# Kernel tuning notes

Measured on AMD Instinct MI355X. Metric: run time of the kernel, lower is better.

The kernel has to match this reference:

```python
import jax, jax.numpy as jnp
import numpy as np
import math

NEG_INF = -1e9  # keras Softmax masking uses a large negative additive constant

def setup_inputs() -> dict:
    key = jax.random.key(0)
    k1, k2, k3, k4 = jax.random.split(key, 4)
    B, T, C, H = 4, 4096, 1024, 128
    x = jax.random.normal(k1, (B, T, C), dtype=jnp.float32)
    Wq = jax.random.normal(k2, (C, H), dtype=jnp.float32) * (1.0 / math.sqrt(C))
    Wk = jax.random.normal(k3, (C, H), dtype=jnp.float32) * (1.0 / math.sqrt(C))
    Wv = jax.random.normal(k4, (C, H), dtype=jnp.float32) * (1.0 / math.sqrt(C))
    return {"x": x, "Wq": Wq, "Wk": Wk, "Wv": Wv}

def reference(x, Wq, Wk, Wv):
    # x: [B, T, C]; projections are bias-free Dense layers
    B, T, C = x.shape
    q = jnp.einsum('btc,ch->bth', x, Wq)  # [B, T, H]
    k = jnp.einsum('btc,ch->bth', x, Wk)  # [B, T, H]
    v = jnp.einsum('btc,ch->bth', x, Wv)  # [B, T, H]
    # NOTE: original scales by sqrt(C) (the input channel dim), not sqrt(head_size)
    wei = jnp.einsum('bth,bsh->bts', q, k) / math.sqrt(C)  # [B, T, T]
    causal = jnp.tril(jnp.ones((T, T), dtype=bool))
    wei = jnp.where(causal[None, :, :], wei, NEG_INF)
    wei = jax.nn.softmax(wei, axis=-1)
    # dropout is identity at inference
    out = jnp.einsum('bts,bsh->bth', wei, v)  # [B, T, H]
    return out
```

## Files before the change

kernel.cpp:

```cpp
#include <hip/hip_runtime.h>
#include <hip/hip_bf16.h>

typedef __bf16 bf16x8 __attribute__((ext_vector_type(8)));
typedef __bf16 bf16x4 __attribute__((ext_vector_type(4)));
typedef float  f32x4  __attribute__((ext_vector_type(4)));

#define NB 4
#define TT 4096
#define CC 1024
#define HH 128
#define PS 72
#define MNEG -30000.0f

__device__ inline void gload16(const void* g, void* l) {
  __builtin_amdgcn_global_load_lds(
      (const __attribute__((address_space(1))) void*)g,
      (__attribute__((address_space(3))) void*)l, 16, 0, 0);
}

__global__ void detect_dtype(const unsigned int* __restrict__ xw, int* __restrict__ flag) {
  int t = threadIdx.x;
  int cnt = 0;
#pragma unroll
  for (int i = 0; i < 4; ++i) {
    unsigned int w = xw[t + 64 * i];
    int e = (int)((w >> 7) & 0xFFu);
    cnt += (e >= 100 && e <= 135) ? 1 : 0;
  }
  cnt += __shfl_xor(cnt, 1);  cnt += __shfl_xor(cnt, 2);  cnt += __shfl_xor(cnt, 4);
  cnt += __shfl_xor(cnt, 8);  cnt += __shfl_xor(cnt, 16); cnt += __shfl_xor(cnt, 32);
  if (t == 0) *flag = (cnt >= 128) ? 1 : 0;
}

__global__ __launch_bounds__(256) void transpose_w3(
    const void* __restrict__ Wq, const void* __restrict__ Wk,
    const void* __restrict__ Wv, __bf16* __restrict__ Wt,
    const int* __restrict__ flagp) {
  int isbf = *flagp;
  int which = blockIdx.y;
  const void* W = (which == 0) ? Wq : (which == 1) ? Wk : Wv;
  int idx = blockIdx.x * 256 + threadIdx.x;
  int h = idx & 127, c = idx >> 7;
  __bf16 val;
  if (isbf) val = ((const __bf16*)W)[c * HH + h];
  else      val = (__bf16)(((const float*)W)[c * HH + h]);
  size_t o = (size_t)(c >> 6) * 24576 + (size_t)which * 8192 +
             (size_t)((c >> 3) & 7) * 1024 + (size_t)h * 8 + (c & 7);
  Wt[o] = val;
}

__global__ __launch_bounds__(768) void qkv_proj(
    const void* __restrict__ x, const __bf16* __restrict__ Wt,
    __bf16* __restrict__ q, __bf16* __restrict__ ktl, __bf16* __restrict__ vtl,
    const int* __restrict__ flagp) {
  __shared__ __align__(16) __bf16 XT[2][4096];
  __shared__ __align__(16) __bf16 WTs[2][24576];
  int isbf = *flagp;
  int tid = threadIdx.x, lane = tid & 63, wave = tid >> 6;
  int which = wave >> 2, rowgrp = wave & 3;
  int l16 = lane & 15, quad = lane >> 4;
  int row0 = blockIdx.x * 64;
  f32x4 acc[8] = {};

#define STAGE(ss, b)                                                          \
  for (int i = wave; i < 56; i += 12) {                                       \
    if (i < 8) {                                                              \
      int row = i * 8 + (lane >> 3), g = lane & 7;                            \
      bf16x8 pk;                                                              \
      if (isbf) {                                                             \
        pk = *(const bf16x8*)((const __bf16*)x + (size_t)(row0 + row) * CC +  \
                              (ss) * 64 + g * 8);                             \
      } else {                                                                \
        const float* xf = (const float*)x + (size_t)(row0 + row) * CC +       \
                          (ss) * 64 + g * 8;                                  \
        f32x4 lo = *(const f32x4*)xf;                                         \
        f32x4 hi = *(const f32x4*)(xf + 4);                                   \
        for (int j = 0; j < 4; ++j) { pk[j] = (__bf16)lo[j]; pk[j+4] = (__bf16)hi[j]; } \
      }                                                                       \
      *(bf16x8*)(&XT[b][g * 512 + (row ^ g) * 8]) = pk;                       \
    } else {                                                                  \
      int j = i - 8;                                                          \
      gload16(Wt + (size_t)(ss) * 24576 + j * 512 + lane * 8,                 \
              &WTs[b][j * 512]);                                              \
    }                                                                         \
  }

  STAGE(0, 0);
  for (int s = 0; s < 16; ++s) {
    int cb = s & 1;
    __syncthreads();
    if (s + 1 < 16) { STAGE(s + 1, cb ^ 1); }
#pragma unroll
    for (int t = 0; t < 2; ++t) {
      int g = t * 4 + quad;
      bf16x8 a = *(const bf16x8*)(&XT[cb][g * 512 + ((rowgrp * 16 + l16) ^ g) * 8]);
#pragma unroll
      for (int nt = 0; nt < 8; ++nt) {
        bf16x8 b = *(const bf16x8*)(&WTs[cb][(size_t)which * 8192 + g * 1024 + (nt * 16 + l16) * 8]);
        acc[nt] = __builtin_amdgcn_mfma_f32_16x16x32_bf16(a, b, acc[nt], 0, 0, 0);
      }
    }
  }
#undef STAGE

  int tile = row0 >> 6;
  if (which == 0) {
#pragma unroll
    for (int nt = 0; nt < 8; ++nt)
#pragma unroll
      for (int r = 0; r < 4; ++r) {
        int row = row0 + rowgrp * 16 + quad * 4 + r;
        q[(size_t)row * HH + nt * 16 + l16] = (__bf16)acc[nt][r];
      }
  } else if (which == 1) {
    __bf16* kb = ktl + (size_t)tile * 8192;
#pragma unroll
    for (int nt = 0; nt < 8; ++nt) {
      int h = nt * 16 + l16, g = h >> 3, j = h & 7;
#pragma unroll
      for (int r = 0; r < 4; ++r) {
        int sidx = rowgrp * 16 + quad * 4 + r;
        kb[g * 512 + sidx * 8 + j] = (__bf16)acc[nt][r];
      }
    }
  } else {
    __bf16* vb = vtl + (size_t)tile * 8192;
#pragma unroll
    for (int nt = 0; nt < 8; ++nt) {
      int h = nt * 16 + l16;
      int sb = rowgrp * 16 + quad * 4;
      bf16x4 pk;
#pragma unroll
      for (int r = 0; r < 4; ++r) pk[r] = (__bf16)acc[nt][r];
      *(bf16x4*)(vb + (sb >> 3) * 1024 + h * 8 + (sb & 7)) = pk;
    }
  }
}

__global__ __launch_bounds__(768, 3) void flash_attn(
    const __bf16* __restrict__ q, const __bf16* __restrict__ ktl,
    const __bf16* __restrict__ vtl, void* __restrict__ out,
    const int* __restrict__ flagp) {
  __shared__ __align__(16) __bf16 PL[12][16 * PS];
  __shared__ float CMB[4][32][132];
  __shared__ float CL[4][32];

  int bx = blockIdx.x;
  int batch = (bx & 7) >> 1;
  int qt0 = ((bx >> 3) << 1) | (bx & 1);

  int tid = threadIdx.x, lane = tid & 63, wave = tid >> 6;
  int p = wave >> 1, rowgrp = wave & 1;
  int l16 = lane & 15, quad = lane >> 4;

  int kA = (6 * (qt0 + 1) + 32) / 65;
  kA = max(1, min(5, kA));
  int unit, kg, nkg, qtu, rh;
  if (p < kA) { unit = 0; kg = p;      nkg = kA;     qtu = qt0;      rh = 0; }
  else        { unit = 1; kg = p - kA; nkg = 6 - kA; qtu = 63 - qt0; rh = 1; }

  int qb = qtu * 64;
  int rb = rh * 32 + rowgrp * 16;
  const __bf16* qp  = q   + (size_t)batch * TT * HH;
  const __bf16* ktb = ktl + (size_t)batch * TT * HH;
  const __bf16* vtb = vtl + (size_t)batch * TT * HH;

  bf16x8 qf[4];
  {
    const __bf16* qrow = qp + (size_t)(qb + rb + l16) * HH + quad * 8;
#pragma unroll
    for (int ks = 0; ks < 4; ++ks) qf[ks] = *(const bf16x8*)(qrow + ks * 32);
  }
  bf16x8 onesf;
#pragma unroll
  for (int j = 0; j < 8; ++j) onesf[j] = (l16 == 0) ? (__bf16)1.0f : (__bf16)0.0f;

  f32x4 acc_o[8] = {};
  f32x4 acc_l = {};
  const float SC = 0.0450842200278f;
  const float M0 = 4.0f;
  int qrl = qb + rb + quad * 4;

  for (int jt = kg; jt <= qtu; jt += nkg) {
    const __bf16* kt  = ktb + (size_t)jt * 8192;
    const __bf16* vt2 = vtb + (size_t)jt * 8192;

    bf16x8 kf[4][4];
#pragma unroll
    for (int ks = 0; ks < 4; ++ks)
#pragma unroll
      for (int kn = 0; kn < 4; ++kn)
        kf[ks][kn] = *(const bf16x8*)(kt + ((4 * ks + quad) * 64 + kn * 16 + l16) * 8);

    f32x4 accs[4] = {};
#pragma unroll
    for (int ks = 0; ks < 4; ++ks)
#pragma unroll
      for (int kn = 0; kn < 4; ++kn)
        accs[kn] = __builtin_amdgcn_mfma_f32_16x16x32_bf16(qf[ks], kf[ks][kn], accs[kn], 0, 0, 0);

    bf16x8 vf[2][8];
#pragma unroll
    for (int ks2 = 0; ks2 < 2; ++ks2)
#pragma unroll
      for (int nt = 0; nt < 8; ++nt)
        vf[ks2][nt] = *(const bf16x8*)(vt2 + (ks2 * 4 + quad) * 1024 + (nt * 16 + l16) * 8);

    float pv[4][4];
    if (jt == qtu) {
#pragma unroll
      for (int nt = 0; nt < 4; ++nt) {
        int kcol = jt * 64 + nt * 16 + l16;
#pragma unroll
        for (int r = 0; r < 4; ++r) {
          float z = fmaf(accs[nt][r], SC, -M0);
          z = (kcol <= qrl + r) ? z : MNEG;
          pv[nt][r] = exp2f(z);
        }
      }
    } else {
#pragma unroll
      for (int nt = 0; nt < 4; ++nt)
#pragma unroll
        for (int r = 0; r < 4; ++r)
          pv[nt][r] = exp2f(fmaf(accs[nt][r], SC, -M0));
    }

    __bf16* pw = &PL[wave][0];
#pragma unroll
    for (int nt = 0; nt < 4; ++nt)
#pragma unroll
      for (int r = 0; r < 4; ++r)
        pw[(quad * 4 + r) * PS + nt * 16 + l16] = (__bf16)pv[nt][r];

#pragma unroll
    for (int ks2 = 0; ks2 < 2; ++ks2) {
      bf16x8 pa = *(const bf16x8*)(pw + l16 * PS + ks2 * 32 + quad * 8);
      acc_l = __builtin_amdgcn_mfma_f32_16x16x32_bf16(pa, onesf, acc_l, 0, 0, 0);
#pragma unroll
      for (int nt = 0; nt < 8; ++nt)
        acc_o[nt] = __builtin_amdgcn_mfma_f32_16x16x32_bf16(pa, vf[ks2][nt], acc_o[nt], 0, 0, 0);
    }
  }

  int rr = rowgrp * 16 + quad * 4;
  if (kg > 0) {
    int slot = (unit == 0) ? (kg - 1) : (kA - 1 + kg - 1);
#pragma unroll
    for (int nt = 0; nt < 8; ++nt)
#pragma unroll
      for (int r = 0; r < 4; ++r)
        CMB[slot][rr + r][nt * 16 + l16] = acc_o[nt][r];
    if (l16 == 0) {
#pragma unroll
      for (int r = 0; r < 4; ++r) CL[slot][rr + r] = acc_l[r];
    }
  }
  __syncthreads();
  if (kg == 0) {
    int lo  = (unit == 0) ? 0 : kA - 1;
    int cnt = (unit == 0) ? kA - 1 : 5 - kA;
    int isbf = *flagp;
    __bf16* ob = (__bf16*)out + (size_t)batch * TT * HH;
    float*  of = (float*)out  + (size_t)batch * TT * HH;
    float inv[4];
#pragma unroll
    for (int r = 0; r < 4; ++r) {
      float lr = __shfl(acc_l[r], lane & 48);
      for (int c = 0; c < cnt; ++c) lr += CL[lo + c][rr + r];
      inv[r] = 1.f / fmaxf(lr, 1e-30f);
    }
#pragma unroll
    for (int nt = 0; nt < 8; ++nt)
#pragma unroll
      for (int r = 0; r < 4; ++r) {
        int row = qb + rh * 32 + rr + r;
        int col = nt * 16 + l16;
        float val = acc_o[nt][r];
        for (int c = 0; c < cnt; ++c) val += CMB[lo + c][rr + r][col];
        val *= inv[r];
        size_t idx = (size_t)row * HH + col;
        if (isbf) ob[idx] = (__bf16)val;
        else      of[idx] = val;
      }
  }
}

extern "C" void kernel_launch(void* const* d_in, const int* in_sizes, int n_in,
                              void* d_out, int out_size, void* d_ws, size_t ws_size,
                              hipStream_t stream) {
  const void* x  = d_in[0];
  const void* Wq = d_in[1];
  const void* Wk = d_in[2];
  const void* Wv = d_in[3];
  char* wsb = (char*)d_ws;
  __bf16* q   = (__bf16*)wsb;
  __bf16* ktl = q   + (size_t)NB * TT * HH;
  __bf16* vtl = ktl + (size_t)NB * TT * HH;
  __bf16* wt  = vtl + (size_t)NB * TT * HH;
  size_t base = (((size_t)(3 * NB * TT * HH + 3 * CC * HH) * 2) + 255) & ~(size_t)255;
  int* flag = (int*)(wsb + base);
  (void)ws_size; (void)in_sizes; (void)n_in; (void)out_size;

  detect_dtype<<<1, 64, 0, stream>>>((const unsigned int*)x, flag);
  transpose_w3<<<dim3(512, 3), 256, 0, stream>>>(Wq, Wk, Wv, wt, flag);
  qkv_proj<<<256, 768, 0, stream>>>(x, wt, q, ktl, vtl, flag);
  flash_attn<<<NB * 64, 768, 0, stream>>>(q, ktl, vtl, d_out, flag);
}
```

Before: 175.3 us.

## Split wave pair work by key columns and head halves with shared P tile

Each pair of waves now covers all 32 query rows but splits the S tile's key columns and the output head dimension in half. Each wave loads only half the K and V fragments per tile and shares the P tile through double-buffered LDS, with a __syncthreads per iteration. The loop now runs a uniform trip count across the block, with masked zero-contribution iterations for waves that have fewer tiles. This is meant to halve per-wave global K/V fragment traffic and register pressure, at the cost of block-wide barriers and some wasted padded iterations.

```diff
diff --git a/kernel.cpp b/kernel.cpp
--- a/kernel.cpp
+++ b/kernel.cpp
@@ -141,7 +141,7 @@
     const __bf16* __restrict__ q, const __bf16* __restrict__ ktl,
     const __bf16* __restrict__ vtl, void* __restrict__ out,
     const int* __restrict__ flagp) {
-  __shared__ __align__(16) __bf16 PL[12][16 * PS];
+  __shared__ __align__(16) __bf16 PLs[6][2][32 * PS];
   __shared__ float CMB[4][32][132];
   __shared__ float CL[4][32];
 
@@ -150,110 +150,142 @@
   int qt0 = ((bx >> 3) << 1) | (bx & 1);
 
   int tid = threadIdx.x, lane = tid & 63, wave = tid >> 6;
-  int p = wave >> 1, rowgrp = wave & 1;
+  int p = wave >> 1, rw = wave & 1;
   int l16 = lane & 15, quad = lane >> 4;
 
   int kA = (6 * (qt0 + 1) + 32) / 65;
   kA = max(1, min(5, kA));
-  int unit, kg, nkg, qtu, rh;
-  if (p < kA) { unit = 0; kg = p;      nkg = kA;     qtu = qt0;      rh = 0; }
-  else        { unit = 1; kg = p - kA; nkg = 6 - kA; qtu = 63 - qt0; rh = 1; }
+  int qtB = 63 - qt0;
+  int unit, kg, nkg, qtu, rbase;
+  if (p < kA) { unit = 0; kg = p;      nkg = kA;     qtu = qt0; rbase = 0;  }
+  else        { unit = 1; kg = p - kA; nkg = 6 - kA; qtu = qtB; rbase = 32; }
 
   int qb = qtu * 64;
-  int rb = rh * 32 + rowgrp * 16;
+  int MAXT = max(qt0 / kA + 1, qtB / (6 - kA) + 1);
+  int mytrips = (qtu - kg) / nkg + 1;
+
   const __bf16* qp  = q   + (size_t)batch * TT * HH;
   const __bf16* ktb = ktl + (size_t)batch * TT * HH;
   const __bf16* vtb = vtl + (size_t)batch * TT * HH;
 
-  bf16x8 qf[4];
-  {
-    const __bf16* qrow = qp + (size_t)(qb + rb + l16) * HH + quad * 8;
-#pragma unroll
-    for (int ks = 0; ks < 4; ++ks) qf[ks] = *(const bf16x8*)(qrow + ks * 32);
+  bf16x8 qf[2][4];
+#pragma unroll
+  for (int rg = 0; rg < 2; ++rg) {
+    const __bf16* qrow = qp + (size_t)(qb + rbase + rg * 16 + l16) * HH + quad * 8;
+#pragma unroll
+    for (int ks = 0; ks < 4; ++ks) qf[rg][ks] = *(const bf16x8*)(qrow + ks * 32);
   }
   bf16x8 onesf;
 #pragma unroll
   for (int j = 0; j < 8; ++j) onesf[j] = (l16 == 0) ? (__bf16)1.0f : (__bf16)0.0f;
 
-  f32x4 acc_o[8] = {};
-  f32x4 acc_l = {};
+  f32x4 acc_o[2][4] = {};
+  f32x4 acc_l[2] = {};
   const float SC = 0.0450842200278f;
   const float M0 = 4.0f;
-  int qrl = qb + rb + quad * 4;
-
-  for (int jt = kg; jt <= qtu; jt += nkg) {
-    const __bf16* kt  = ktb + (size_t)jt * 8192;
-    const __bf16* vt2 = vtb + (size_t)jt * 8192;
-
-    bf16x8 kf[4][4];
+
+  for (int t = 0; t < MAXT; ++t) {
+    int jt = kg + t * nkg;
+    int valid = (t < mytrips);
+    int jtc = valid ? jt : kg;
+    const __bf16* kt  = ktb + (size_t)jtc * 8192;
+    const __bf16* vt2 = vtb + (size_t)jtc * 8192;
+
+    bf16x8 kf[4][2];
 #pragma unroll
     for (int ks = 0; ks < 4; ++ks)
 #pragma unroll
-      for (int kn = 0; kn < 4; ++kn)
-        kf[ks][kn] = *(const bf16x8*)(kt + ((4 * ks + quad) * 64 + kn * 16 + l16) * 8);
-
-    f32x4 accs[4] = {};
+      for (int kn = 0; kn < 2; ++kn)
+        kf[ks][kn] = *(const bf16x8*)(kt + ((4 * ks + quad) * 64 + (rw * 2 + kn) * 16 + l16) * 8);
+
+    f32x4 accs[2][2] = {};
 #pragma unroll
     for (int ks = 0; ks < 4; ++ks)
 #pragma unroll
-      for (int kn = 0; kn < 4; ++kn)
-        accs[kn] = __builtin_amdgcn_mfma_f32_16x16x32_bf16(qf[ks], kf[ks][kn], accs[kn], 0, 0, 0);
-
-    bf16x8 vf[2][8];
+      for (int rg = 0; rg < 2; ++rg)
+#pragma unroll
+        for (int kn = 0; kn < 2; ++kn)
+          accs[rg][kn] = __builtin_amdgcn_mfma_f32_16x16x32_bf16(qf[rg][ks], kf[ks][kn], accs[rg][kn], 0, 0, 0);
+
+    bf16x8 vf[2][4];
 #pragma unroll
     for (int ks2 = 0; ks2 < 2; ++ks2)
 #pragma unroll
-      for (int nt = 0; nt < 8; ++nt)
-        vf[ks2][nt] = *(const bf16x8*)(vt2 + (ks2 * 4 + quad) * 1024 + (nt * 16 + l16) * 8);
-
-    float pv[4][4];
-    if (jt == qtu) {
+      for (int nt = 0; nt < 4; ++nt)
+        vf[ks2][nt] = *(const bf16x8*)(vt2 + (ks2 * 4 + quad) * 1024 + (rw * 64 + nt * 16 + l16) * 8);
+
+    float pv[2][2][4];
+    if (valid && jt == qtu) {
+#pragma unroll
+      for (int rg = 0; rg < 2; ++rg)
+#pragma unroll
+        for (int kn = 0; kn < 2; ++kn) {
+          int kcol = jt * 64 + (rw * 2 + kn) * 16 + l16;
+          int qr0 = qb + rbase + rg * 16 + quad * 4;
+#pragma unroll
+          for (int r = 0; r < 4; ++r) {
+            float z = fmaf(accs[rg][kn][r], SC, -M0);
+            z = (kcol <= qr0 + r) ? z : MNEG;
+            pv[rg][kn][r] = exp2f(z);
+          }
+        }
+    } else if (valid) {
+#pragma unroll
+      for (int rg = 0; rg < 2; ++rg)
+#pragma unroll
+        for (int kn = 0; kn < 2; ++kn)
+#pragma unroll
+          for (int r = 0; r < 4; ++r)
+            pv[rg][kn][r] = exp2f(fmaf(accs[rg][kn][r], SC, -M0));
+    } else {
+#pragma unroll
+      for (int rg = 0; rg < 2; ++rg)
+#pragma unroll
+        for (int kn = 0; kn < 2; ++kn)
+#pragma unroll
+          for (int r = 0; r < 4; ++r)
+            pv[rg][kn][r] = 0.0f;
+    }
+
+    __bf16* pw = &PLs[p][t & 1][0];
+#pragma unroll
+    for (int rg = 0; rg < 2; ++rg)
+#pragma unroll
+      for (int kn = 0; kn < 2; ++kn)
+#pragma unroll
+        for (int r = 0; r < 4; ++r)
+          pw[(rg * 16 + quad * 4 + r) * PS + (rw * 2 + kn) * 16 + l16] = (__bf16)pv[rg][kn][r];
+
+    __syncthreads();
+
+#pragma unroll
+    for (int ks2 = 0; ks2 < 2; ++ks2) {
+      bf16x8 pa0 = *(const bf16x8*)(pw + l16 * PS + ks2 * 32 + quad * 8);
+      bf16x8 pa1 = *(const bf16x8*)(pw + (16 + l16) * PS + ks2 * 32 + quad * 8);
+      acc_l[0] = __builtin_amdgcn_mfma_f32_16x16x32_bf16(pa0, onesf, acc_l[0], 0, 0, 0);
+      acc_l[1] = __builtin_amdgcn_mfma_f32_16x16x32_bf16(pa1, onesf, acc_l[1], 0, 0, 0);
 #pragma unroll
       for (int nt = 0; nt < 4; ++nt) {
-        int kcol = jt * 64 + nt * 16 + l16;
-#pragma unroll
-        for (int r = 0; r < 4; ++r) {
-          float z = fmaf(accs[nt][r], SC, -M0);
-          z = (kcol <= qrl + r) ? z : MNEG;
-          pv[nt][r] = exp2f(z);
-        }
-      }
-    } else {
-#pragma unroll
-      for (int nt = 0; nt < 4; ++nt)
-#pragma unroll
-        for (int r = 0; r < 4; ++r)
-          pv[nt][r] = exp2f(fmaf(accs[nt][r], SC, -M0));
-    }
-
-    __bf16* pw = &PL[wave][0];
-#pragma unroll
-    for (int nt = 0; nt < 4; ++nt)
-#pragma unroll
-      for (int r = 0; r < 4; ++r)
-        pw[(quad * 4 + r) * PS + nt * 16 + l16] = (__bf16)pv[nt][r];
-
-#pragma unroll
-    for (int ks2 = 0; ks2 < 2; ++ks2) {
-      bf16x8 pa = *(const bf16x8*)(pw + l16 * PS + ks2 * 32 + quad * 8);
-      acc_l = __builtin_amdgcn_mfma_f32_16x16x32_bf16(pa, onesf, acc_l, 0, 0, 0);
-#pragma unroll
-      for (int nt = 0; nt < 8; ++nt)
-        acc_o[nt] = __builtin_amdgcn_mfma_f32_16x16x32_bf16(pa, vf[ks2][nt], acc_o[nt], 0, 0, 0);
-    }
-  }
-
-  int rr = rowgrp * 16 + quad * 4;
+        acc_o[0][nt] = __builtin_amdgcn_mfma_f32_16x16x32_bf16(pa0, vf[ks2][nt], acc_o[0][nt], 0, 0, 0);
+        acc_o[1][nt] = __builtin_amdgcn_mfma_f32_16x16x32_bf16(pa1, vf[ks2][nt], acc_o[1][nt], 0, 0, 0);
+      }
+    }
+  }
+
   if (kg > 0) {
     int slot = (unit == 0) ? (kg - 1) : (kA - 1 + kg - 1);
 #pragma unroll
-    for (int nt = 0; nt < 8; ++nt)
-#pragma unroll
-      for (int r = 0; r < 4; ++r)
-        CMB[slot][rr + r][nt * 16 + l16] = acc_o[nt][r];
-    if (l16 == 0) {
-#pragma unroll
-      for (int r = 0; r < 4; ++r) CL[slot][rr + r] = acc_l[r];
+    for (int rh = 0; rh < 2; ++rh)
+#pragma unroll
+      for (int nt = 0; nt < 4; ++nt)
+#pragma unroll
+        for (int r = 0; r < 4; ++r)
+          CMB[slot][rh * 16 + quad * 4 + r][rw * 64 + nt * 16 + l16] = acc_o[rh][nt][r];
+    if (rw == 0 && l16 == 0) {
+#pragma unroll
+      for (int rh = 0; rh < 2; ++rh)
+#pragma unroll
+        for (int r = 0; r < 4; ++r) CL[slot][rh * 16 + quad * 4 + r] = acc_l[rh][r];
     }
   }
   __syncthreads();
@@ -263,26 +295,29 @@
     int isbf = *flagp;
     __bf16* ob = (__bf16*)out + (size_t)batch * TT * HH;
     float*  of = (float*)out  + (size_t)batch * TT * HH;
-    float inv[4];
-#pragma unroll
-    for (int r = 0; r < 4; ++r) {
-      float lr = __shfl(acc_l[r], lane & 48);
-      for (int c = 0; c < cnt; ++c) lr += CL[lo + c][rr + r];
-      inv[r] = 1.f / fmaxf(lr, 1e-30f);
-    }
-#pragma unroll
-    for (int nt = 0; nt < 8; ++nt)
+#pragma unroll
+    for (int rh = 0; rh < 2; ++rh) {
+      float inv[4];
 #pragma unroll
       for (int r = 0; r < 4; ++r) {
-        int row = qb + rh * 32 + rr + r;
-        int col = nt * 16 + l16;
-        float val = acc_o[nt][r];
-        for (int c = 0; c < cnt; ++c) val += CMB[lo + c][rr + r][col];
-        val *= inv[r];
-        size_t idx = (size_t)row * HH + col;
-        if (isbf) ob[idx] = (__bf16)val;
-        else      of[idx] = val;
-      }
+        float lr = __shfl(acc_l[rh][r], lane & 48);
+        for (int c = 0; c < cnt; ++c) lr += CL[lo + c][rh * 16 + quad * 4 + r];
+        inv[r] = 1.f / fmaxf(lr, 1e-30f);
+      }
+#pragma unroll
+      for (int nt = 0; nt < 4; ++nt)
+#pragma unroll
+        for (int r = 0; r < 4; ++r) {
+          int row = qb + rbase + rh * 16 + quad * 4 + r;
+          int col = rw * 64 + nt * 16 + l16;
+          float val = acc_o[rh][nt][r];
+          for (int c = 0; c < cnt; ++c) val += CMB[lo + c][rh * 16 + quad * 4 + r][col];
+          val *= inv[r];
+          size_t idx = (size_t)row * HH + col;
+          if (isbf) ob[idx] = (__bf16)val;
+          else      of[idx] = val;
+        }
+    }
   }
 }
 
```

After: 173.6 us. No clear change (-1.0%).
